# Kernel optimization log

Hardware: AMD Instinct MI355X
Metric: run time of the kernel (lower is better)

The kernel has to match this reference:

```python
import jax, jax.numpy as jnp
import numpy as np

DIM = 1024
HEADS = 16
GROUPS = 4
DIM_HEAD = 64
INNER = HEADS * DIM_HEAD  # 1024
KV_DIM = 2 * DIM_HEAD * GROUPS  # 512
B, N = 4, 2048
EPS = 1e-6


def _layernorm(x, scale, bias, eps=EPS):
    mu = jnp.mean(x, axis=-1, keepdims=True)
    var = jnp.mean(jnp.square(x - mu), axis=-1, keepdims=True)
    return (x - mu) * jax.lax.rsqrt(var + eps) * scale + bias


def setup_inputs() -> dict:
    key = jax.random.key(0)
    ks = jax.random.split(key, 10)
    lecun = lambda k, shape: jax.random.normal(k, shape, jnp.float32) * (1.0 / np.sqrt(shape[0]))
    return {
        "x": jax.random.normal(ks[0], (B, N, DIM), jnp.float32),
        "ln_scale": jnp.ones((DIM,), jnp.float32),
        "ln_bias": jnp.zeros((DIM,), jnp.float32),
        "Wq": lecun(ks[1], (DIM, INNER)),
        "Wkv": lecun(ks[2], (DIM, KV_DIM)),
        "qn_scale": jnp.ones((DIM_HEAD,), jnp.float32),
        "qn_bias": jnp.zeros((DIM_HEAD,), jnp.float32),
        "kn_scale": jnp.ones((DIM_HEAD,), jnp.float32),
        "kn_bias": jnp.zeros((DIM_HEAD,), jnp.float32),
        "Wout": lecun(ks[3], (INNER, DIM)),
    }


def reference(x, ln_scale, ln_bias, Wq, Wkv, qn_scale, qn_bias, kn_scale, kn_bias, Wout):
    b, n, _ = x.shape
    g, hg, d = GROUPS, HEADS // GROUPS, DIM_HEAD
    scale = d ** -0.5
    xn = _layernorm(x, ln_scale, ln_bias)
    # q: (b,n,inner) -> (b,h,n,d)
    q = (xn @ Wq).reshape(b, n, HEADS, d).transpose(0, 2, 1, 3)
    kv = xn @ Wkv
    k, v = jnp.split(kv, 2, axis=-1)
    # (b,n,g*d) -> (b,g,n,d)
    k = k.reshape(b, n, g, d).transpose(0, 2, 1, 3)
    v = v.reshape(b, n, g, d).transpose(0, 2, 1, 3)
    q = _layernorm(q, qn_scale, qn_bias)
    k = _layernorm(k, kn_scale, kn_bias)
    # split heads into groups: (b, g*hg, n, d) -> (b, g, hg, n, d)
    qg = q.reshape(b, g, hg, n, d)
    dots = jnp.einsum('bghqd,bgkd->bghqk', qg, k) * scale
    attn = jax.nn.softmax(dots, axis=-1)
    out = jnp.einsum('bghqk,bgkd->bghqd', attn, v)  # (b,g,hg,n,d)
    out = out.transpose(0, 3, 1, 2, 4).reshape(b, n, g * hg * d)
    return out @ Wout
```

## Files before the change

kernel.cpp:

```cpp
#include <hip/hip_runtime.h>
#include <cstdint>
#include <cstddef>

typedef unsigned short u16;
typedef __attribute__((ext_vector_type(4))) float f32x4;
typedef __attribute__((ext_vector_type(8))) __bf16 bf16x8;
typedef __attribute__((ext_vector_type(4))) __bf16 bf16x4;
typedef __attribute__((ext_vector_type(8))) unsigned short u16x8;

#define DEV static __device__ __forceinline__

#if __has_builtin(__builtin_amdgcn_exp2f)
#define EXP2(x) __builtin_amdgcn_exp2f(x)
#else
#define EXP2(x) exp2f(x)
#endif

DEV float bf2f(u16 v) { return __uint_as_float(((unsigned)v) << 16); }
DEV u16 f2bf(float f) {
  unsigned u = __float_as_uint(f);
  return (u16)((u + 0x7FFFu + ((u >> 16) & 1u)) >> 16);
}

DEV void gl_lds16(const void* g, void* l) {
  __builtin_amdgcn_global_load_lds((const __attribute__((address_space(1))) void*)g,
                                   (__attribute__((address_space(3))) void*)l, 16, 0, 0);
}

__global__ __launch_bounds__(256) void transpose64(const float* __restrict__ in,
                                                   u16* __restrict__ out, int incols) {
  __shared__ __attribute__((aligned(16))) u16 t[64 * 72];
  const int r0 = blockIdx.x * 64, c0 = blockIdx.y * 64, tid = threadIdx.x;
#pragma unroll
  for (int i = 0; i < 2; i++) {
    int c = i * 256 + tid;
    int row = c >> 3, cc = c & 7;
    const float* src = &in[(size_t)(r0 + row) * incols + c0 + cc * 8];
    f32x4 v0 = *(const f32x4*)src;
    f32x4 v1 = *(const f32x4*)(src + 4);
    u16x8 o;
#pragma unroll
    for (int j = 0; j < 4; j++) { o[j] = f2bf(v0[j]); o[4 + j] = f2bf(v1[j]); }
    *(u16x8*)&t[row * 72 + cc * 8] = o;
  }
  __syncthreads();
#pragma unroll
  for (int i = 0; i < 2; i++) {
    int c = i * 256 + tid;
    int d = c >> 3, nc = c & 7;
    u16x8 o;
#pragma unroll
    for (int j = 0; j < 8; j++) o[j] = t[(nc * 8 + j) * 72 + d];
    *(u16x8*)&out[(size_t)(c0 + d) * 1024 + r0 + nc * 8] = o;
  }
}

__global__ __launch_bounds__(256) void ln_x(const float* __restrict__ x,
                                            const float* __restrict__ sc,
                                            const float* __restrict__ bi,
                                            u16* __restrict__ xn) {
  __shared__ float red[8];
  const int row = blockIdx.x, tid = threadIdx.x;
  const int w = tid >> 6;
  f32x4 f = *(const f32x4*)&x[(size_t)row * 1024 + tid * 4];
  float s = f[0] + f[1] + f[2] + f[3];
  float q = f[0] * f[0] + f[1] * f[1] + f[2] * f[2] + f[3] * f[3];
#pragma unroll
  for (int off = 1; off < 64; off <<= 1) {
    s += __shfl_xor(s, off);
    q += __shfl_xor(q, off);
  }
  if ((tid & 63) == 0) { red[w] = s; red[4 + w] = q; }
  __syncthreads();
  float S = red[0] + red[1] + red[2] + red[3];
  float Q = red[4] + red[5] + red[6] + red[7];
  float mu = S * (1.0f / 1024.0f);
  float var = Q * (1.0f / 1024.0f) - mu * mu;
  float rs = rsqrtf(var + 1e-6f);
  f32x4 scv = *(const f32x4*)&sc[tid * 4];
  f32x4 biv = *(const f32x4*)&bi[tid * 4];
  u16* o = xn + (size_t)row * 1024 + tid * 4;
#pragma unroll
  for (int j = 0; j < 4; j++) o[j] = f2bf((f[j] - mu) * rs * scv[j] + biv[j]);
}

template <bool F32OUT>
__global__ __launch_bounds__(256) void gemm_bt(const u16* __restrict__ A,
                                               const u16* __restrict__ Bt,
                                               void* __restrict__ Cp,
                                               int M, int N, int K) {
  __shared__ __attribute__((aligned(16))) u16 Als[128 * 64];
  __shared__ __attribute__((aligned(16))) u16 Bls[128 * 64];
  const int tid = threadIdx.x;
  const int w = tid >> 6, lane = tid & 63, ln = lane & 15, quad = lane >> 4;
  const int m0 = blockIdx.y * 128, n0 = blockIdx.x * 128;
  const int moff = (w & 1) * 64, noff = (w >> 1) * 64;
  const f32x4 fzero = {0.f, 0.f, 0.f, 0.f};
  f32x4 acc[4][4];
#pragma unroll
  for (int i = 0; i < 4; i++)
#pragma unroll
    for (int j = 0; j < 4; j++) acc[i][j] = fzero;

  const u16* aS[4];
  const u16* bS[4];
#pragma unroll
  for (int i = 0; i < 4; i++) {
    int s = i * 256 + tid;
    int row = s >> 3, cs = (s & 7) ^ (row & 7);
    aS[i] = A + (size_t)(m0 + row) * K + cs * 8;
    bS[i] = Bt + (size_t)(n0 + row) * K + cs * 8;
  }

  for (int k0 = 0; k0 < K; k0 += 64) {
    __syncthreads();
#pragma unroll
    for (int i = 0; i < 4; i++) {
      int s = i * 256 + tid;
      gl_lds16(aS[i] + k0, &Als[s * 8]);
      gl_lds16(bS[i] + k0, &Bls[s * 8]);
    }
    __syncthreads();
#pragma unroll
    for (int kk = 0; kk < 2; kk++) {
      bf16x8 af[4], bfv[4];
#pragma unroll
      for (int mi = 0; mi < 4; mi++)
        af[mi] = *(const bf16x8*)
            &Als[(moff + mi * 16 + ln) * 64 + (((kk * 4 + quad) ^ (ln & 7)) * 8)];
#pragma unroll
      for (int ni = 0; ni < 4; ni++)
        bfv[ni] = *(const bf16x8*)
            &Bls[(noff + ni * 16 + ln) * 64 + (((kk * 4 + quad) ^ (ln & 7)) * 8)];
#pragma unroll
      for (int mi = 0; mi < 4; mi++)
#pragma unroll
        for (int ni = 0; ni < 4; ni++)
          acc[mi][ni] = __builtin_amdgcn_mfma_f32_16x16x32_bf16(af[mi], bfv[ni],
                                                                acc[mi][ni], 0, 0, 0);
    }
  }
#pragma unroll
  for (int mi = 0; mi < 4; mi++)
#pragma unroll
    for (int ni = 0; ni < 4; ni++)
#pragma unroll
      for (int r = 0; r < 4; r++) {
        size_t m = m0 + moff + mi * 16 + quad * 4 + r;
        size_t n = n0 + noff + ni * 16 + ln;
        if (F32OUT)
          ((float*)Cp)[m * N + n] = acc[mi][ni][r];
        else
          ((u16*)Cp)[m * N + n] = f2bf(acc[mi][ni][r]);
      }
}

__global__ __launch_bounds__(256) void qk_ln(const u16* __restrict__ qkv,
                                             const float* __restrict__ qs,
                                             const float* __restrict__ qb,
                                             const float* __restrict__ ks,
                                             const float* __restrict__ kb,
                                             u16* __restrict__ Q,
                                             u16* __restrict__ Kb) {
  const float SCL = 0.18033688011112042f;
  const int m = blockIdx.x;
  const int b = m >> 11, n = m & 2047;
  const int tid = threadIdx.x, w = tid >> 6, lane = tid & 63;
  const u16* rowp = qkv + (size_t)m * 1536;
  const float qsc = qs[lane], qbi = qb[lane];
  const float ksc = ks[lane], kbi = kb[lane];
#pragma unroll
  for (int i = 0; i < 4; i++) {
    int h = w * 4 + i;
    float v = bf2f(rowp[h * 64 + lane]);
    float s = v, q2 = v * v;
#pragma unroll
    for (int off = 1; off < 64; off <<= 1) {
      s += __shfl_xor(s, off);
      q2 += __shfl_xor(q2, off);
    }
    float mu = s * (1.0f / 64.0f);
    float var = q2 * (1.0f / 64.0f) - mu * mu;
    float y = ((v - mu) * rsqrtf(var + 1e-6f) * qsc + qbi) * SCL;
    Q[((size_t)(b * 16 + h) * 2048 + n) * 64 + lane] = f2bf(y);
  }
  {
    int g = w;
    float v = bf2f(rowp[1024 + g * 64 + lane]);
    float s = v, q2 = v * v;
#pragma unroll
    for (int off = 1; off < 64; off <<= 1) {
      s += __shfl_xor(s, off);
      q2 += __shfl_xor(q2, off);
    }
    float mu = s * (1.0f / 64.0f);
    float var = q2 * (1.0f / 64.0f) - mu * mu;
    float y = (v - mu) * rsqrtf(var + 1e-6f) * ksc + kbi;
    Kb[((size_t)(b * 4 + g) * 2048 + n) * 64 + lane] = f2bf(y);
  }
}

__global__ __launch_bounds__(256) void vtrans(const u16* __restrict__ qkv,
                                              u16* __restrict__ Vt) {
  __shared__ __attribute__((aligned(16))) u16 t[64 * 72];
  const int n0 = blockIdx.x * 64;
  const int bg = blockIdx.y;
  const int b = bg >> 2, g = bg & 3;
  const int tid = threadIdx.x;
  const u16* src = qkv + (size_t)(b * 2048 + n0) * 1536 + 1280 + g * 64;
#pragma unroll
  for (int i = 0; i < 2; i++) {
    int c = i * 256 + tid;
    int row = c >> 3, cc = c & 7;
    *(f32x4*)&t[row * 72 + cc * 8] = *(const f32x4*)&src[(size_t)row * 1536 + cc * 8];
  }
  __syncthreads();
  u16* dst = Vt + (size_t)bg * 64 * 2048 + n0;
#pragma unroll
  for (int i = 0; i < 2; i++) {
    int c = i * 256 + tid;
    int d = c >> 3, nc = c & 7;
    u16x8 o;
#pragma unroll
    for (int j = 0; j < 8; j++) o[j] = t[(nc * 8 + j) * 72 + d];
    *(u16x8*)&dst[(size_t)d * 2048 + nc * 8] = o;
  }
}

__global__ __launch_bounds__(256) void attn(const u16* __restrict__ Q,
                                            const u16* __restrict__ Kb,
                                            const u16* __restrict__ Vt,
                                            u16* __restrict__ Out) {
  __shared__ __attribute__((aligned(16))) u16 Kls[64 * 64];
  __shared__ __attribute__((aligned(16))) u16 Vls[64 * 64];
  __shared__ __attribute__((aligned(16))) u16 Pls[4][32 * 64];
  const int qt = blockIdx.x;
  const int bh = blockIdx.y;
  const int b = bh >> 4, h = bh & 15, g = h >> 2;
  const int tid = threadIdx.x, w = tid >> 6, lane = tid & 63;
  const int ln = lane & 15, quad = lane >> 4;
  const u16* Qg = Q + ((size_t)(b * 16 + h) * 2048 + qt * 128 + w * 32) * 64;
  const u16* Kg = Kb + (size_t)(b * 4 + g) * 2048 * 64;
  const u16* Vg = Vt + (size_t)(b * 4 + g) * 64 * 2048;
  const f32x4 fzero = {0.f, 0.f, 0.f, 0.f};

  bf16x8 qf[2][2];
#pragma unroll
  for (int mi = 0; mi < 2; mi++)
#pragma unroll
    for (int ks2 = 0; ks2 < 2; ks2++)
      qf[mi][ks2] = *(const bf16x8*)&Qg[(size_t)(mi * 16 + ln) * 64 + ks2 * 32 + quad * 8];

  f32x4 oacc[4][2];
#pragma unroll
  for (int ni = 0; ni < 4; ni++)
#pragma unroll
    for (int mi = 0; mi < 2; mi++) oacc[ni][mi] = fzero;
  float lsum[2] = {0.f, 0.f};
  u16* Pw = &Pls[w][0];

  const int sk0 = tid, sk1 = 256 + tid;
  const int krow0 = sk0 >> 3, kcs0 = (sk0 & 7) ^ (krow0 & 7);
  const int krow1 = sk1 >> 3, kcs1 = (sk1 & 7) ^ (krow1 & 7);

  for (int kt = 0; kt < 32; kt++) {
    __syncthreads();
    gl_lds16(Kg + (size_t)(kt * 64 + krow0) * 64 + kcs0 * 8, &Kls[sk0 * 8]);
    gl_lds16(Kg + (size_t)(kt * 64 + krow1) * 64 + kcs1 * 8, &Kls[sk1 * 8]);
    gl_lds16(Vg + (size_t)krow0 * 2048 + kt * 64 + kcs0 * 8, &Vls[sk0 * 8]);
    gl_lds16(Vg + (size_t)krow1 * 2048 + kt * 64 + kcs1 * 8, &Vls[sk1 * 8]);
    __syncthreads();

    f32x4 sacc[2][4];
#pragma unroll
    for (int ni = 0; ni < 4; ni++) {
      const int krow = ni * 16 + ln;
      bf16x8 kf0 = *(const bf16x8*)&Kls[krow * 64 + ((quad ^ (ln & 7)) * 8)];
      bf16x8 kf1 = *(const bf16x8*)&Kls[krow * 64 + (((4 + quad) ^ (ln & 7)) * 8)];
#pragma unroll
      for (int mi = 0; mi < 2; mi++) {
        f32x4 tt = __builtin_amdgcn_mfma_f32_16x16x32_bf16(kf0, qf[mi][0], fzero, 0, 0, 0);
        sacc[mi][ni] = __builtin_amdgcn_mfma_f32_16x16x32_bf16(kf1, qf[mi][1], tt, 0, 0, 0);
      }
    }

#pragma unroll
    for (int mi = 0; mi < 2; mi++) {
      float ls = 0.f;
      const int mrow = mi * 16 + ln;
#pragma unroll
      for (int ni = 0; ni < 4; ni++) {
        float p0 = EXP2(sacc[mi][ni][0]);
        float p1 = EXP2(sacc[mi][ni][1]);
        float p2 = EXP2(sacc[mi][ni][2]);
        float p3 = EXP2(sacc[mi][ni][3]);
        ls += (p0 + p1) + (p2 + p3);
        bf16x4 pv = {(__bf16)p0, (__bf16)p1, (__bf16)p2, (__bf16)p3};
        char* dst = (char*)&Pw[mrow * 64] +
                    (((2 * ni + (quad >> 1)) ^ (ln & 7)) * 16) + ((quad & 1) * 8);
        *(bf16x4*)dst = pv;
      }
      ls += __shfl_xor(ls, 16);
      ls += __shfl_xor(ls, 32);
      lsum[mi] += ls;
    }

#pragma unroll
    for (int kc = 0; kc < 2; kc++) {
      bf16x8 pf[2];
#pragma unroll
      for (int mi = 0; mi < 2; mi++)
        pf[mi] = *(const bf16x8*)
            &Pw[(mi * 16 + ln) * 64 + (((4 * kc + quad) ^ (ln & 7)) * 8)];
#pragma unroll
      for (int ni = 0; ni < 4; ni++) {
        const int drow = ni * 16 + ln;
        bf16x8 vf = *(const bf16x8*)&Vls[drow * 64 + (((4 * kc + quad) ^ (ln & 7)) * 8)];
#pragma unroll
        for (int mi = 0; mi < 2; mi++)
          oacc[ni][mi] = __builtin_amdgcn_mfma_f32_16x16x32_bf16(vf, pf[mi],
                                                                 oacc[ni][mi], 0, 0, 0);
      }
    }
  }

#pragma unroll
  for (int mi = 0; mi < 2; mi++) {
    float inv = 1.0f / lsum[mi];
    u16* Og = Out + ((size_t)b * 2048 + qt * 128 + w * 32 + mi * 16 + ln) * 1024 + h * 64;
#pragma unroll
    for (int ni = 0; ni < 4; ni++) {
      bf16x4 ov = {(__bf16)(oacc[ni][mi][0] * inv), (__bf16)(oacc[ni][mi][1] * inv),
                   (__bf16)(oacc[ni][mi][2] * inv), (__bf16)(oacc[ni][mi][3] * inv)};
      *(bf16x4*)&Og[ni * 16 + quad * 4] = ov;
    }
  }
}

extern "C" void kernel_launch(void* const* d_in, const int* in_sizes, int n_in,
                              void* d_out, int out_size, void* d_ws, size_t ws_size,
                              hipStream_t stream) {
  const float* x    = (const float*)d_in[0];
  const float* lns  = (const float*)d_in[1];
  const float* lnb  = (const float*)d_in[2];
  const float* Wq   = (const float*)d_in[3];
  const float* Wkv  = (const float*)d_in[4];
  const float* qns  = (const float*)d_in[5];
  const float* qnb  = (const float*)d_in[6];
  const float* kns  = (const float*)d_in[7];
  const float* knb  = (const float*)d_in[8];
  const float* Wout = (const float*)d_in[9];
  float* out = (float*)d_out;
  char* ws = (char*)d_ws;

  const size_t o_xn  = 0;
  const size_t o_qkv = 16777216;
  const size_t o_bt  = o_qkv + 25165824;
  const size_t o_k   = o_bt + 3145728;
  const size_t o_vt  = o_k + 4194304;
  u16* xn   = (u16*)(ws + o_xn);
  u16* qkv  = (u16*)(ws + o_qkv);
  u16* bt   = (u16*)(ws + o_bt);
  u16* Kbuf = (u16*)(ws + o_k);
  u16* Vtb  = (u16*)(ws + o_vt);
  u16* Qbuf = xn;
  u16* aout = qkv;

  transpose64<<<dim3(16, 16), 256, 0, stream>>>(Wq, bt, 1024);
  transpose64<<<dim3(16, 8), 256, 0, stream>>>(Wkv, bt + 1024 * 1024, 512);
  ln_x<<<8192, 256, 0, stream>>>(x, lns, lnb, xn);
  gemm_bt<false><<<dim3(12, 64), 256, 0, stream>>>(xn, bt, qkv, 8192, 1536, 1024);
  transpose64<<<dim3(16, 16), 256, 0, stream>>>(Wout, bt, 1024);
  qk_ln<<<8192, 256, 0, stream>>>(qkv, qns, qnb, kns, knb, Qbuf, Kbuf);
  vtrans<<<dim3(32, 16), 256, 0, stream>>>(qkv, Vtb);
  attn<<<dim3(16, 64), 256, 0, stream>>>(Qbuf, Kbuf, Vtb, aout);
  gemm_bt<true><<<dim3(8, 64), 256, 0, stream>>>(aout, bt, out, 8192, 1024, 1024);

  (void)in_sizes; (void)n_in; (void)out_size; (void)ws_size;
}
```

Before: 291.8 us.

## Double-buffer K/V tiles and keep softmax probabilities in registers

The attention kernel now double-buffers K and V tiles in LDS, prefetching the next tile while computing on the current one, with one barrier per iteration instead of two. The P matrix no longer goes through LDS: the exp outputs are packed directly into MFMA B-operand registers, and the V fragment reads are permuted to match that k ordering. It also sets a min-blocks-per-SM launch bound of 4. The aim is to hide global-load latency and drop the LDS round-trip for P, at the cost of more LDS for the second buffer and possible register pressure.

```diff
diff --git a/kernel.cpp b/kernel.cpp
--- a/kernel.cpp
+++ b/kernel.cpp
@@ -227,13 +227,14 @@
   }
 }
 
-__global__ __launch_bounds__(256) void attn(const u16* __restrict__ Q,
-                                            const u16* __restrict__ Kb,
-                                            const u16* __restrict__ Vt,
-                                            u16* __restrict__ Out) {
-  __shared__ __attribute__((aligned(16))) u16 Kls[64 * 64];
-  __shared__ __attribute__((aligned(16))) u16 Vls[64 * 64];
-  __shared__ __attribute__((aligned(16))) u16 Pls[4][32 * 64];
+__global__ __launch_bounds__(256, 4) void attn(const u16* __restrict__ Q,
+                                               const u16* __restrict__ Kb,
+                                               const u16* __restrict__ Vt,
+                                               u16* __restrict__ Out) {
+  __shared__ __attribute__((aligned(16))) u16 Kls0[64 * 64];
+  __shared__ __attribute__((aligned(16))) u16 Kls1[64 * 64];
+  __shared__ __attribute__((aligned(16))) u16 Vls0[64 * 64];
+  __shared__ __attribute__((aligned(16))) u16 Vls1[64 * 64];
   const int qt = blockIdx.x;
   const int bh = blockIdx.y;
   const int b = bh >> 4, h = bh & 15, g = h >> 2;
@@ -257,26 +258,27 @@
 #pragma unroll
     for (int mi = 0; mi < 2; mi++) oacc[ni][mi] = fzero;
   float lsum[2] = {0.f, 0.f};
-  u16* Pw = &Pls[w][0];
 
   const int sk0 = tid, sk1 = 256 + tid;
   const int krow0 = sk0 >> 3, kcs0 = (sk0 & 7) ^ (krow0 & 7);
   const int krow1 = sk1 >> 3, kcs1 = (sk1 & 7) ^ (krow1 & 7);
 
-  for (int kt = 0; kt < 32; kt++) {
-    __syncthreads();
-    gl_lds16(Kg + (size_t)(kt * 64 + krow0) * 64 + kcs0 * 8, &Kls[sk0 * 8]);
-    gl_lds16(Kg + (size_t)(kt * 64 + krow1) * 64 + kcs1 * 8, &Kls[sk1 * 8]);
-    gl_lds16(Vg + (size_t)krow0 * 2048 + kt * 64 + kcs0 * 8, &Vls[sk0 * 8]);
-    gl_lds16(Vg + (size_t)krow1 * 2048 + kt * 64 + kcs1 * 8, &Vls[sk1 * 8]);
-    __syncthreads();
+  auto STAGE = [&](int kt, u16* Kd, u16* Vd) {
+    gl_lds16(Kg + (size_t)(kt * 64 + krow0) * 64 + kcs0 * 8, &Kd[sk0 * 8]);
+    gl_lds16(Kg + (size_t)(kt * 64 + krow1) * 64 + kcs1 * 8, &Kd[sk1 * 8]);
+    gl_lds16(Vg + (size_t)krow0 * 2048 + kt * 64 + kcs0 * 8, &Vd[sk0 * 8]);
+    gl_lds16(Vg + (size_t)krow1 * 2048 + kt * 64 + kcs1 * 8, &Vd[sk1 * 8]);
+  };
+
+  auto BODY = [&](int kt, const u16* K_, const u16* V_, u16* Kn, u16* Vn) {
+    if (kt + 1 < 32) STAGE(kt + 1, Kn, Vn);
 
     f32x4 sacc[2][4];
 #pragma unroll
     for (int ni = 0; ni < 4; ni++) {
       const int krow = ni * 16 + ln;
-      bf16x8 kf0 = *(const bf16x8*)&Kls[krow * 64 + ((quad ^ (ln & 7)) * 8)];
-      bf16x8 kf1 = *(const bf16x8*)&Kls[krow * 64 + (((4 + quad) ^ (ln & 7)) * 8)];
+      bf16x8 kf0 = *(const bf16x8*)&K_[krow * 64 + ((quad ^ (ln & 7)) * 8)];
+      bf16x8 kf1 = *(const bf16x8*)&K_[krow * 64 + (((4 + quad) ^ (ln & 7)) * 8)];
 #pragma unroll
       for (int mi = 0; mi < 2; mi++) {
         f32x4 tt = __builtin_amdgcn_mfma_f32_16x16x32_bf16(kf0, qf[mi][0], fzero, 0, 0, 0);
@@ -284,10 +286,10 @@
       }
     }
 
+    bf16x8 pfa[2][2];
 #pragma unroll
     for (int mi = 0; mi < 2; mi++) {
       float ls = 0.f;
-      const int mrow = mi * 16 + ln;
 #pragma unroll
       for (int ni = 0; ni < 4; ni++) {
         float p0 = EXP2(sacc[mi][ni][0]);
@@ -295,10 +297,11 @@
         float p2 = EXP2(sacc[mi][ni][2]);
         float p3 = EXP2(sacc[mi][ni][3]);
         ls += (p0 + p1) + (p2 + p3);
-        bf16x4 pv = {(__bf16)p0, (__bf16)p1, (__bf16)p2, (__bf16)p3};
-        char* dst = (char*)&Pw[mrow * 64] +
-                    (((2 * ni + (quad >> 1)) ^ (ln & 7)) * 16) + ((quad & 1) * 8);
-        *(bf16x4*)dst = pv;
+        const int e = (ni & 1) * 4;
+        pfa[mi][ni >> 1][e + 0] = (__bf16)p0;
+        pfa[mi][ni >> 1][e + 1] = (__bf16)p1;
+        pfa[mi][ni >> 1][e + 2] = (__bf16)p2;
+        pfa[mi][ni >> 1][e + 3] = (__bf16)p3;
       }
       ls += __shfl_xor(ls, 16);
       ls += __shfl_xor(ls, 32);
@@ -307,21 +310,28 @@
 
 #pragma unroll
     for (int kc = 0; kc < 2; kc++) {
-      bf16x8 pf[2];
-#pragma unroll
-      for (int mi = 0; mi < 2; mi++)
-        pf[mi] = *(const bf16x8*)
-            &Pw[(mi * 16 + ln) * 64 + (((4 * kc + quad) ^ (ln & 7)) * 8)];
 #pragma unroll
       for (int ni = 0; ni < 4; ni++) {
-        const int drow = ni * 16 + ln;
-        bf16x8 vf = *(const bf16x8*)&Vls[drow * 64 + (((4 * kc + quad) ^ (ln & 7)) * 8)];
+        const int base = (ni * 16 + ln) * 64 + (quad & 1) * 4;
+        bf16x4 va = *(const bf16x4*)&V_[base + (((4 * kc + (quad >> 1)) ^ (ln & 7)) * 8)];
+        bf16x4 vb = *(const bf16x4*)&V_[base + (((4 * kc + 2 + (quad >> 1)) ^ (ln & 7)) * 8)];
+        bf16x8 vf;
+        vf[0] = va[0]; vf[1] = va[1]; vf[2] = va[2]; vf[3] = va[3];
+        vf[4] = vb[0]; vf[5] = vb[1]; vf[6] = vb[2]; vf[7] = vb[3];
 #pragma unroll
         for (int mi = 0; mi < 2; mi++)
-          oacc[ni][mi] = __builtin_amdgcn_mfma_f32_16x16x32_bf16(vf, pf[mi],
+          oacc[ni][mi] = __builtin_amdgcn_mfma_f32_16x16x32_bf16(vf, pfa[mi][kc],
                                                                  oacc[ni][mi], 0, 0, 0);
       }
     }
+    __syncthreads();
+  };
+
+  STAGE(0, Kls0, Vls0);
+  __syncthreads();
+  for (int kt = 0; kt < 32; kt += 2) {
+    BODY(kt, Kls0, Vls0, Kls1, Vls1);
+    BODY(kt + 1, Kls1, Vls1, Kls0, Vls0);
   }
 
 #pragma unroll
```

New measurement: 289.8 us. About the same (-0.7%).
